# Kernel optimization log

Hardware: AMD Instinct MI355X
Metric: run time of the kernel (lower is better)

## Reference

```python
import jax, jax.numpy as jnp
import numpy as np

BETA = 0.25
SCALE_NUM = 4  # len(latents_scale)


def setup_inputs() -> dict:
    key = jax.random.key(0)
    kz, ke = jax.random.split(key)
    z = jax.random.normal(kz, (8, 256, 32, 32), dtype=jnp.float32)
    emb_weight = jax.random.normal(ke, (16384, 256), dtype=jnp.float32) * 0.02
    return {"z": z, "emb_weight": emb_weight}


def reference(z, emb_weight):
    # z: [B, C, H, W] with C == vq_embed_dim and H == W (source reshapes with W twice)
    B, C, H, W = z.shape
    z_det = jax.lax.stop_gradient(z)

    # NOTE: in the source, `residual` is flattened ONCE before the scale loop and
    # never updated inside it, so every scale picks the same indices. We compute
    # the nearest-codebook assignment once (identical math, argmin of cdist is
    # invariant under sqrt, so squared distances suffice).
    residual = jnp.transpose(z_det, (0, 2, 3, 1)).reshape(-1, C)  # [N, D], N=B*H*W
    d2 = (jnp.sum(residual * residual, axis=1, keepdims=True)
          - 2.0 * residual @ emb_weight.T
          + jnp.sum(emb_weight * emb_weight, axis=1))  # [N, n_e]
    idx = jnp.argmin(d2, axis=1).reshape(B, W, W)  # [B, W, W]

    quantized = jnp.transpose(emb_weight[idx], (0, 3, 1, 2))  # [B, C, H, W]

    z_hat = jnp.zeros_like(z_det)
    loss = jnp.float32(0.0)
    for _ in range(SCALE_NUM):
        z_hat = z_hat + quantized
        loss = loss + BETA * jnp.mean((jax.lax.stop_gradient(z_hat) - z) ** 2) \
                    + jnp.mean((z_hat - z_det) ** 2)
    loss = loss / SCALE_NUM

    total_idx = jnp.concatenate([idx] * SCALE_NUM, axis=1)  # [B, SCALE_NUM*W, W]
    z_hat_out = z + jax.lax.stop_gradient(z_hat - z)  # straight-through
    return z_hat_out, loss, total_idx
```

## Files before the change

### kernel.cpp

```cpp
#include <hip/hip_runtime.h>

#define D      256
#define N_E    16384
#define NPTS   8192
#define ZOUT   2097152
#define MARGIN 2.0e-2f
#define STRIPS 4

typedef short bf16x8 __attribute__((ext_vector_type(8)));
typedef unsigned short us8 __attribute__((ext_vector_type(8)));
typedef float f32x16 __attribute__((ext_vector_type(16)));
typedef unsigned long long u64;

__device__ __forceinline__ unsigned short f2bf(float x) {
    unsigned int u = __float_as_uint(x);
    return (unsigned short)((u + 0x7FFFu + ((u >> 16) & 1u)) >> 16);
}
__device__ __forceinline__ void gl_lds16(const void* g, void* l) {
    __builtin_amdgcn_global_load_lds(
        (const __attribute__((address_space(1))) unsigned int*)g,
        (__attribute__((address_space(3))) unsigned int*)l, 16, 0, 0);
}

__global__ __launch_bounds__(256) void prep(
    const float* __restrict__ z, const float* __restrict__ emb,
    unsigned short* __restrict__ Zpk, float* __restrict__ Zf32,
    unsigned short* __restrict__ Epk, float* __restrict__ e2) {
    const int t = threadIdx.x;
    if (blockIdx.x < 256) {
        const int n0 = blockIdx.x * 32;
        const int p = t & 31, ks8 = t >> 5;
        const int n = n0 + p;
        const int b = n >> 10, hw = n & 1023;
        const float* zb = z + (size_t)b * 262144 + hw;
        const int k0 = ks8 * 32;
        float v[32];
        #pragma unroll
        for (int kk = 0; kk < 32; ++kk)
            v[kk] = zb[(size_t)(k0 + kk) * 1024];
        #pragma unroll
        for (int i = 0; i < 8; ++i) {
            float4 f = {v[i * 4], v[i * 4 + 1], v[i * 4 + 2], v[i * 4 + 3]};
            *(float4*)(Zf32 + (size_t)n * D + k0 + i * 4) = f;
        }
        const int g = n >> 5;
        #pragma unroll
        for (int i = 0; i < 4; ++i) {
            us8 hv;
            #pragma unroll
            for (int c = 0; c < 8; ++c) hv[c] = f2bf(-2.0f * v[i * 8 + c]);
            const int kabs = k0 + i * 8;
            const int ks = kabs >> 4;
            const int l = (n & 31) + ((kabs >> 3) & 1) * 32;
            *(us8*)(Zpk + ((size_t)(g * 16 + ks) * 64 + l) * 8) = hv;
        }
    } else {
        const int j0 = (blockIdx.x - 256) * 32;
        const int jj = j0 + (t >> 3), q = t & 7;
        const float* row = emb + (size_t)jj * D + q * 32;
        float v[32];
        float s = 0.f;
        #pragma unroll
        for (int i = 0; i < 8; ++i) {
            const float4 x = *(const float4*)(row + i * 4);
            v[i * 4] = x.x; v[i * 4 + 1] = x.y; v[i * 4 + 2] = x.z; v[i * 4 + 3] = x.w;
            s += x.x * x.x + x.y * x.y + x.z * x.z + x.w * x.w;
        }
        const int g = jj >> 5;
        #pragma unroll
        for (int i = 0; i < 4; ++i) {
            us8 hv;
            #pragma unroll
            for (int c = 0; c < 8; ++c) hv[c] = f2bf(v[i * 8 + c]);
            const int kabs = q * 32 + i * 8;
            const int ks = kabs >> 4;
            const int l = (jj & 31) + ((kabs >> 3) & 1) * 32;
            *(us8*)(Epk + ((size_t)(g * 16 + ks) * 64 + l) * 8) = hv;
        }
        s += __shfl_xor(s, 1);
        s += __shfl_xor(s, 2);
        s += __shfl_xor(s, 4);
        if (q == 0) e2[jj] = s;
    }
}

__global__ __launch_bounds__(256, 2) void mfma_gemm(
    const unsigned short* __restrict__ Epk, const unsigned short* __restrict__ Zpk,
    const float* __restrict__ e2, float* __restrict__ tminv,
    u64* __restrict__ tmask) {
    __shared__ unsigned short Zbuf[64 * 512];

    const int tid = threadIdx.x, lane = tid & 63, wid = tid >> 6;
    const int c32 = lane & 31, l5 = lane >> 5;
    const int n0 = blockIdx.x * 128;
    const int cs0 = blockIdx.y * (STRIPS * 256);

    #pragma unroll
    for (int ks = 0; ks < 16; ++ks)
        gl_lds16(Zpk + ((size_t)((n0 >> 5) + wid) * 16 + ks) * 512 + lane * 8,
                 Zbuf + (wid * 16 + ks) * 512);
    __syncthreads();

    for (int s = 0; s < STRIPS; ++s) {
        const int cb = cs0 + s * 256 + wid * 64;
        const unsigned short* eb = Epk + ((size_t)(cb >> 5) * 16) * 512 + lane * 8;
        const unsigned short* zb = Zbuf + lane * 8;

        f32x16 acc[2][4];
        const f32x16 z16 = {0.f};
        #pragma unroll
        for (int i = 0; i < 2; ++i)
            #pragma unroll
            for (int j = 0; j < 4; ++j) acc[i][j] = z16;

        bf16x8 ec[2], pc[4];
        ec[0] = *(const bf16x8*)(eb);
        ec[1] = *(const bf16x8*)(eb + 16 * 512);
        #pragma unroll
        for (int j = 0; j < 4; ++j) pc[j] = *(const bf16x8*)(zb + (j * 16) * 512);

        #pragma unroll 4
        for (int ks = 0; ks < 16; ++ks) {
            bf16x8 en[2], pn[4];
            if (ks < 15) {
                en[0] = *(const bf16x8*)(eb + (ks + 1) * 512);
                en[1] = *(const bf16x8*)(eb + (16 + ks + 1) * 512);
                #pragma unroll
                for (int j = 0; j < 4; ++j)
                    pn[j] = *(const bf16x8*)(zb + (j * 16 + ks + 1) * 512);
            }
            #pragma unroll
            for (int i = 0; i < 2; ++i)
                #pragma unroll
                for (int j = 0; j < 4; ++j)
                    acc[i][j] = __builtin_amdgcn_mfma_f32_32x32x16_bf16(
                        ec[i], pc[j], acc[i][j], 0, 0, 0);
            if (ks < 15) {
                ec[0] = en[0]; ec[1] = en[1];
                #pragma unroll
                for (int j = 0; j < 4; ++j) pc[j] = pn[j];
            }
        }

        float e2r[2][16];
        #pragma unroll
        for (int i = 0; i < 2; ++i)
            #pragma unroll
            for (int r = 0; r < 16; ++r)
                e2r[i][r] = e2[cb + i * 32 + (r & 3) + 8 * (r >> 2) + 4 * l5];
        #pragma unroll
        for (int j = 0; j < 4; ++j) {
            float m = e2r[0][0] + acc[0][j][0];
            #pragma unroll
            for (int r = 1; r < 16; ++r) m = fminf(m, e2r[0][r] + acc[0][j][r]);
            #pragma unroll
            for (int r = 0; r < 16; ++r) m = fminf(m, e2r[1][r] + acc[1][j][r]);
            m = fminf(m, __shfl_xor(m, 32));
            const float th = m + MARGIN;
            unsigned mk[2];
            #pragma unroll
            for (int i = 0; i < 2; ++i) {
                unsigned mm = 0;
                #pragma unroll
                for (int r = 0; r < 16; ++r) {
                    const int row = (r & 3) + 8 * (r >> 2) + 4 * l5;
                    mm |= (e2r[i][r] + acc[i][j][r] <= th) ? (1u << row) : 0u;
                }
                mk[i] = mm | (unsigned)__shfl_xor((int)mm, 32);
            }
            if (l5 == 0) {
                const int pt = n0 + j * 32 + c32;
                const int g = cb >> 6;
                tminv[(size_t)g * NPTS + pt] = m;
                tmask[(size_t)g * NPTS + pt] =
                    ((u64)mk[1] << 32) | (u64)mk[0];
            }
        }
    }
}

__global__ __launch_bounds__(256) void rescore(
    const float* __restrict__ tminv, const u64* __restrict__ tmask,
    const float* __restrict__ Zf32, const float* __restrict__ emb,
    const float* __restrict__ e2, int* __restrict__ idxf,
    float* __restrict__ out_idx, float* __restrict__ loss) {
    __shared__ float sm[256 * 5];
    const int tid = threadIdx.x, lane = tid & 63, w = tid >> 6;
    const int n0 = blockIdx.x * 4;
    const int n = n0 + w;
    if (blockIdx.x == 0 && tid == 0) loss[0] = 0.f;

    {
        const float4 v = *(const float4*)(tminv + (size_t)tid * NPTS + n0);
        sm[tid * 5 + 0] = v.x; sm[tid * 5 + 1] = v.y;
        sm[tid * 5 + 2] = v.z; sm[tid * 5 + 3] = v.w;
    }
    const float4 zr = *(const float4*)(Zf32 + (size_t)n * D + lane * 4);
    __syncthreads();

    float tva[4];
    #pragma unroll
    for (int k = 0; k < 4; ++k) tva[k] = sm[(k * 64 + lane) * 5 + w];
    float m1 = fminf(fminf(tva[0], tva[1]), fminf(tva[2], tva[3]));
    #pragma unroll
    for (int st = 1; st < 64; st <<= 1) m1 = fminf(m1, __shfl_xor(m1, st));
    const float thresh = m1 + MARGIN;

    u64 best = ~0ull;
    #pragma unroll
    for (int k = 0; k < 4; ++k) {
        u64 gm = __ballot(tva[k] <= thresh);
        while (gm) {
            const int bit = (int)__builtin_ctzll(gm);
            gm &= gm - 1;
            const int g = k * 64 + bit;
            u64 cm = tmask[(size_t)g * NPTS + n];
            while (cm) {
                const int r = (int)__builtin_ctzll(cm);
                cm &= cm - 1;
                const int c = g * 64 + r;
                const float4 ev = *(const float4*)(emb + (size_t)c * D + lane * 4);
                float s = zr.x * ev.x + zr.y * ev.y + zr.z * ev.z + zr.w * ev.w;
                #pragma unroll
                for (int st = 1; st < 64; st <<= 1) s += __shfl_xor(s, st);
                const float d = e2[c] - 2.0f * s;
                unsigned int u = __float_as_uint(d);
                u = (u & 0x80000000u) ? ~u : (u | 0x80000000u);
                const u64 key = ((u64)u << 32) | (unsigned int)c;
                if (key < best) best = key;
            }
        }
    }
    if (lane == 0) {
        const int bi = (int)(unsigned int)(best & 0xFFFFFFFFull);
        idxf[n] = bi;
        const int b = n >> 10, hw = n & 1023;
        const float fv = (float)bi;
        #pragma unroll
        for (int sc = 0; sc < 4; ++sc) out_idx[b * 4096 + sc * 1024 + hw] = fv;
    }
}

__global__ __launch_bounds__(256) void quant_loss(
    const float* __restrict__ z, const float* __restrict__ emb,
    const int* __restrict__ idxf, float* __restrict__ out,
    float* __restrict__ loss) {
    __shared__ int idx_l[32];
    __shared__ float wsum[4];
    const int blk = blockIdx.x;
    const int c0 = (blk >> 8) * 64;
    const int rem = blk & 255;
    const int b = rem >> 5, hw0 = (rem & 31) * 32;
    const int t = threadIdx.x, hw_l = t & 31, cg = t >> 5;
    if (t < 32) idx_l[t] = idxf[b * 1024 + hw0 + t];
    __syncthreads();
    const int j = idx_l[hw_l];
    const float* er = emb + (size_t)j * D + c0 + cg * 8;
    const float4 q0 = *(const float4*)er;
    const float4 q1 = *(const float4*)(er + 4);
    const float qv[8] = {q0.x, q0.y, q0.z, q0.w, q1.x, q1.y, q1.z, q1.w};
    float e = 0.f;
    #pragma unroll
    for (int cc = 0; cc < 8; ++cc) {
        const int c = c0 + cg * 8 + cc;
        const size_t zi = (size_t)b * 262144 + (size_t)c * 1024 + hw0 + hw_l;
        const float zv = z[zi];
        const float q = qv[cc];
        const float zh = ((q + q) + q) + q;
        out[zi] = zv + (zh - zv);
        e += 30.0f * q * q - 20.0f * q * zv + 4.0f * zv * zv;
    }
    #pragma unroll
    for (int off = 32; off > 0; off >>= 1) e += __shfl_down(e, off);
    if ((t & 63) == 0) wsum[t >> 6] = e;
    __syncthreads();
    if (t == 0) {
        const float s = wsum[0] + wsum[1] + wsum[2] + wsum[3];
        atomicAdd(loss, s * (0.3125f / 2097152.0f));
    }
}

extern "C" void kernel_launch(void* const* d_in, const int* in_sizes, int n_in,
                              void* d_out, int out_size, void* d_ws, size_t ws_size,
                              hipStream_t stream) {
    const float* z = (const float*)d_in[0];
    const float* emb = (const float*)d_in[1];
    float* out = (float*)d_out;

    unsigned short* Zpk = (unsigned short*)d_ws;
    unsigned short* Epk = Zpk + (size_t)NPTS * D;
    float* Zf32 = (float*)(Epk + (size_t)N_E * D);
    float* e2 = Zf32 + (size_t)NPTS * D;
    float* tminv = e2 + N_E;
    u64* tmask = (u64*)(tminv + (size_t)NPTS * 256);
    int* idxf = (int*)(tmask + (size_t)NPTS * 256);

    float* loss = out + ZOUT;
    float* out_idx = out + ZOUT + 1;

    prep<<<768, 256, 0, stream>>>(z, emb, Zpk, Zf32, Epk, e2);
    mfma_gemm<<<dim3(NPTS / 128, N_E / (256 * STRIPS)), 256, 0, stream>>>(
        Epk, Zpk, e2, tminv, tmask);
    rescore<<<NPTS / 4, 256, 0, stream>>>(tminv, tmask, Zf32, emb, e2, idxf,
                                          out_idx, loss);
    quant_loss<<<1024, 256, 0, stream>>>(z, emb, idxf, out, loss);
}
```

Baseline: 182.5 us.

## Remap GEMM blocks for locality, deepen codebook prefetch, batch rescore points per block

The GEMM grid becomes a flat 1D launch whose block IDs are swizzled so that consecutive blocks share point tiles, aiming at better L2 reuse across chiplets. Codebook fragments are now prefetched two k-steps ahead, the first ones are issued before the LDS barrier and the next strip's are issued during the epilogue, and the k-loop is fully unrolled to hide global load latency. The rescore kernel handles 32 points per block with a transposed, padded shared tile, which cuts block count and gives more coalesced tminv reads. The cost is higher register pressure from the full unroll and more serial work per wave in rescore.

```diff
diff --git a/kernel.cpp b/kernel.cpp
--- a/kernel.cpp
+++ b/kernel.cpp
@@ -92,18 +92,30 @@
 
     const int tid = threadIdx.x, lane = tid & 63, wid = tid >> 6;
     const int c32 = lane & 31, l5 = lane >> 5;
-    const int n0 = blockIdx.x * 128;
-    const int cs0 = blockIdx.y * (STRIPS * 256);
+
+    const int fid = (int)blockIdx.x;
+    const int nid = (fid & 7) * 128 + (fid >> 3);
+    const int bx = nid & 63, by = nid >> 6;
+    const int n0 = bx * 128;
+    const int cs0 = by * (STRIPS * 256);
 
     #pragma unroll
     for (int ks = 0; ks < 16; ++ks)
         gl_lds16(Zpk + ((size_t)((n0 >> 5) + wid) * 16 + ks) * 512 + lane * 8,
                  Zbuf + (wid * 16 + ks) * 512);
+
+    const unsigned short* ebase =
+        Epk + ((size_t)((cs0 >> 5) + wid * 2) * 16) * 512 + lane * 8;
+    bf16x8 ep0 = *(const bf16x8*)(ebase);
+    bf16x8 ep1 = *(const bf16x8*)(ebase + 16 * 512);
+    bf16x8 ep2 = *(const bf16x8*)(ebase + 512);
+    bf16x8 ep3 = *(const bf16x8*)(ebase + 17 * 512);
+
     __syncthreads();
 
     for (int s = 0; s < STRIPS; ++s) {
         const int cb = cs0 + s * 256 + wid * 64;
-        const unsigned short* eb = Epk + ((size_t)(cb >> 5) * 16) * 512 + lane * 8;
+        const unsigned short* eb = ebase + (size_t)s * 65536;
         const unsigned short* zb = Zbuf + lane * 8;
 
         f32x16 acc[2][4];
@@ -113,33 +125,45 @@
             #pragma unroll
             for (int j = 0; j < 4; ++j) acc[i][j] = z16;
 
-        bf16x8 ec[2], pc[4];
-        ec[0] = *(const bf16x8*)(eb);
-        ec[1] = *(const bf16x8*)(eb + 16 * 512);
+        bf16x8 ec0 = ep0, ec1 = ep1;
+        bf16x8 en0 = ep2, en1 = ep3;
+        bf16x8 pc[4], pn[4];
         #pragma unroll
         for (int j = 0; j < 4; ++j) pc[j] = *(const bf16x8*)(zb + (j * 16) * 512);
 
-        #pragma unroll 4
+        #pragma unroll
         for (int ks = 0; ks < 16; ++ks) {
-            bf16x8 en[2], pn[4];
+            const bf16x8 ef0 = ec0, ef1 = ec1;
+            ec0 = en0; ec1 = en1;
+            if (ks < 14) {
+                en0 = *(const bf16x8*)(eb + (ks + 2) * 512);
+                en1 = *(const bf16x8*)(eb + (16 + ks + 2) * 512);
+            }
             if (ks < 15) {
-                en[0] = *(const bf16x8*)(eb + (ks + 1) * 512);
-                en[1] = *(const bf16x8*)(eb + (16 + ks + 1) * 512);
                 #pragma unroll
                 for (int j = 0; j < 4; ++j)
                     pn[j] = *(const bf16x8*)(zb + (j * 16 + ks + 1) * 512);
             }
-            #pragma unroll
-            for (int i = 0; i < 2; ++i)
-                #pragma unroll
-                for (int j = 0; j < 4; ++j)
-                    acc[i][j] = __builtin_amdgcn_mfma_f32_32x32x16_bf16(
-                        ec[i], pc[j], acc[i][j], 0, 0, 0);
+            acc[0][0] = __builtin_amdgcn_mfma_f32_32x32x16_bf16(ef0, pc[0], acc[0][0], 0, 0, 0);
+            acc[0][1] = __builtin_amdgcn_mfma_f32_32x32x16_bf16(ef0, pc[1], acc[0][1], 0, 0, 0);
+            acc[0][2] = __builtin_amdgcn_mfma_f32_32x32x16_bf16(ef0, pc[2], acc[0][2], 0, 0, 0);
+            acc[0][3] = __builtin_amdgcn_mfma_f32_32x32x16_bf16(ef0, pc[3], acc[0][3], 0, 0, 0);
+            acc[1][0] = __builtin_amdgcn_mfma_f32_32x32x16_bf16(ef1, pc[0], acc[1][0], 0, 0, 0);
+            acc[1][1] = __builtin_amdgcn_mfma_f32_32x32x16_bf16(ef1, pc[1], acc[1][1], 0, 0, 0);
+            acc[1][2] = __builtin_amdgcn_mfma_f32_32x32x16_bf16(ef1, pc[2], acc[1][2], 0, 0, 0);
+            acc[1][3] = __builtin_amdgcn_mfma_f32_32x32x16_bf16(ef1, pc[3], acc[1][3], 0, 0, 0);
             if (ks < 15) {
-                ec[0] = en[0]; ec[1] = en[1];
                 #pragma unroll
                 for (int j = 0; j < 4; ++j) pc[j] = pn[j];
             }
+        }
+
+        if (s < STRIPS - 1) {
+            const unsigned short* ebn = eb + 65536;
+            ep0 = *(const bf16x8*)(ebn);
+            ep1 = *(const bf16x8*)(ebn + 16 * 512);
+            ep2 = *(const bf16x8*)(ebn + 512);
+            ep3 = *(const bf16x8*)(ebn + 17 * 512);
         }
 
         float e2r[2][16];
@@ -184,60 +208,67 @@
     const float* __restrict__ Zf32, const float* __restrict__ emb,
     const float* __restrict__ e2, int* __restrict__ idxf,
     float* __restrict__ out_idx, float* __restrict__ loss) {
-    __shared__ float sm[256 * 5];
+    __shared__ float smp[32][257];
     const int tid = threadIdx.x, lane = tid & 63, w = tid >> 6;
-    const int n0 = blockIdx.x * 4;
-    const int n = n0 + w;
+    const int n0 = blockIdx.x * 32;
     if (blockIdx.x == 0 && tid == 0) loss[0] = 0.f;
 
-    {
-        const float4 v = *(const float4*)(tminv + (size_t)tid * NPTS + n0);
-        sm[tid * 5 + 0] = v.x; sm[tid * 5 + 1] = v.y;
-        sm[tid * 5 + 2] = v.z; sm[tid * 5 + 3] = v.w;
-    }
-    const float4 zr = *(const float4*)(Zf32 + (size_t)n * D + lane * 4);
+    #pragma unroll
+    for (int q = 0; q < 8; ++q) {
+        const int g = q * 32 + (tid >> 3);
+        const int pt = (tid & 7) * 4;
+        const float4 v = *(const float4*)(tminv + (size_t)g * NPTS + n0 + pt);
+        smp[pt][g] = v.x; smp[pt + 1][g] = v.y;
+        smp[pt + 2][g] = v.z; smp[pt + 3][g] = v.w;
+    }
     __syncthreads();
 
-    float tva[4];
-    #pragma unroll
-    for (int k = 0; k < 4; ++k) tva[k] = sm[(k * 64 + lane) * 5 + w];
-    float m1 = fminf(fminf(tva[0], tva[1]), fminf(tva[2], tva[3]));
-    #pragma unroll
-    for (int st = 1; st < 64; st <<= 1) m1 = fminf(m1, __shfl_xor(m1, st));
-    const float thresh = m1 + MARGIN;
-
-    u64 best = ~0ull;
-    #pragma unroll
-    for (int k = 0; k < 4; ++k) {
-        u64 gm = __ballot(tva[k] <= thresh);
-        while (gm) {
-            const int bit = (int)__builtin_ctzll(gm);
-            gm &= gm - 1;
-            const int g = k * 64 + bit;
-            u64 cm = tmask[(size_t)g * NPTS + n];
-            while (cm) {
-                const int r = (int)__builtin_ctzll(cm);
-                cm &= cm - 1;
-                const int c = g * 64 + r;
-                const float4 ev = *(const float4*)(emb + (size_t)c * D + lane * 4);
-                float s = zr.x * ev.x + zr.y * ev.y + zr.z * ev.z + zr.w * ev.w;
-                #pragma unroll
-                for (int st = 1; st < 64; st <<= 1) s += __shfl_xor(s, st);
-                const float d = e2[c] - 2.0f * s;
-                unsigned int u = __float_as_uint(d);
-                u = (u & 0x80000000u) ? ~u : (u | 0x80000000u);
-                const u64 key = ((u64)u << 32) | (unsigned int)c;
-                if (key < best) best = key;
-            }
-        }
-    }
-    if (lane == 0) {
-        const int bi = (int)(unsigned int)(best & 0xFFFFFFFFull);
-        idxf[n] = bi;
-        const int b = n >> 10, hw = n & 1023;
-        const float fv = (float)bi;
-        #pragma unroll
-        for (int sc = 0; sc < 4; ++sc) out_idx[b * 4096 + sc * 1024 + hw] = fv;
+    #pragma unroll 1
+    for (int p = 0; p < 8; ++p) {
+        const int ptl = w * 8 + p;
+        const int n = n0 + ptl;
+        const float4 zr = *(const float4*)(Zf32 + (size_t)n * D + lane * 4);
+        float tva[4];
+        #pragma unroll
+        for (int k = 0; k < 4; ++k) tva[k] = smp[ptl][k * 64 + lane];
+        float m1 = fminf(fminf(tva[0], tva[1]), fminf(tva[2], tva[3]));
+        #pragma unroll
+        for (int st = 1; st < 64; st <<= 1) m1 = fminf(m1, __shfl_xor(m1, st));
+        const float thresh = m1 + MARGIN;
+
+        u64 best = ~0ull;
+        #pragma unroll
+        for (int k = 0; k < 4; ++k) {
+            u64 gm = __ballot(tva[k] <= thresh);
+            while (gm) {
+                const int bit = (int)__builtin_ctzll(gm);
+                gm &= gm - 1;
+                const int g = k * 64 + bit;
+                u64 cm = tmask[(size_t)g * NPTS + n];
+                while (cm) {
+                    const int r = (int)__builtin_ctzll(cm);
+                    cm &= cm - 1;
+                    const int c = g * 64 + r;
+                    const float4 ev = *(const float4*)(emb + (size_t)c * D + lane * 4);
+                    float s = zr.x * ev.x + zr.y * ev.y + zr.z * ev.z + zr.w * ev.w;
+                    #pragma unroll
+                    for (int st = 1; st < 64; st <<= 1) s += __shfl_xor(s, st);
+                    const float d = e2[c] - 2.0f * s;
+                    unsigned int u = __float_as_uint(d);
+                    u = (u & 0x80000000u) ? ~u : (u | 0x80000000u);
+                    const u64 key = ((u64)u << 32) | (unsigned int)c;
+                    if (key < best) best = key;
+                }
+            }
+        }
+        if (lane == 0) {
+            const int bi = (int)(unsigned int)(best & 0xFFFFFFFFull);
+            idxf[n] = bi;
+            const int b = n >> 10, hw = n & 1023;
+            const float fv = (float)bi;
+            #pragma unroll
+            for (int sc = 0; sc < 4; ++sc) out_idx[b * 4096 + sc * 1024 + hw] = fv;
+        }
     }
 }
 
@@ -299,9 +330,8 @@
     float* out_idx = out + ZOUT + 1;
 
     prep<<<768, 256, 0, stream>>>(z, emb, Zpk, Zf32, Epk, e2);
-    mfma_gemm<<<dim3(NPTS / 128, N_E / (256 * STRIPS)), 256, 0, stream>>>(
-        Epk, Zpk, e2, tminv, tmask);
-    rescore<<<NPTS / 4, 256, 0, stream>>>(tminv, tmask, Zf32, emb, e2, idxf,
-                                          out_idx, loss);
+    mfma_gemm<<<1024, 256, 0, stream>>>(Epk, Zpk, e2, tminv, tmask);
+    rescore<<<NPTS / 32, 256, 0, stream>>>(tminv, tmask, Zf32, emb, e2, idxf,
+                                           out_idx, loss);
     quant_loss<<<1024, 256, 0, stream>>>(z, emb, idxf, out, loss);
 }
```

After: 301.7 us. 1.65x slower.
